# Kernel tuning notes

Hardware: AMD Instinct MI355X
Metric: run time of the kernel (lower is better)

Reference implementation:

```python
import jax, jax.numpy as jnp
import numpy as np

# ViT-B on the Lorentz hyperboloid (curvature C): points x = [x_time, x_space],
# x_time = sqrt(||x_space||^2 + C). All linear/conv/norm ops act on the space
# part and recompute time; residuals/attention-midpoints renormalize the full
# Lorentz vector back onto the hyperboloid.
B, IMG, P, CIN, D, H, L = 32, 224, 16, 3, 768, 12, 12
HD = D // H          # per-head space dim (64)
DFF = 2048           # swiglu hidden: int(2/3 * 4*768) aligned to 64
C = 1.0
EPS = 1e-6


def _time(xs):
    return jnp.sqrt(jnp.clip(jnp.sum(xs * xs, -1, keepdims=True) + C, EPS, None))


def _to_lorentz(xs):
    return jnp.concatenate([_time(xs), xs], -1)


def _project(z):
    # renormalize full Lorentz vector so <z,z>_L = -C
    zz = jnp.sum(z[..., 1:] ** 2, -1, keepdims=True) - z[..., :1] ** 2
    return z * (jnp.sqrt(C) / jnp.sqrt(jnp.clip(-zz, EPS, None)))


def _lorentz_ln(x, g, b):
    xs = x[..., 1:]
    mu = xs.mean(-1, keepdims=True)
    var = ((xs - mu) ** 2).mean(-1, keepdims=True)
    xs = (xs - mu) / jnp.sqrt(var + 1e-6) * g + b
    return _to_lorentz(xs)


def _lresnet(x, y, w):
    # Lorentzian weighted residual: midpoint of x and w*y, projected to manifold
    return _project(x + w * y)


def _rope_tables():
    # 2D axial rope over the 14x14 patch grid, identity rotation for 1 cls token
    n = IMG // P
    d4 = HD // 4
    inv = 1.0 / (100.0 ** (np.arange(d4) / d4))
    ang = np.arange(n)[:, None] * inv[None, :]            # [n, d4]
    ay = np.repeat(ang[:, None, :], n, axis=1)            # row angles
    ax = np.repeat(ang[None, :, :], n, axis=0)            # col angles
    a = np.concatenate([ay, ax], -1).reshape(n * n, HD // 2)
    cos = np.concatenate([np.ones((1, HD // 2)), np.cos(a)], 0)
    sin = np.concatenate([np.zeros((1, HD // 2)), np.sin(a)], 0)
    return jnp.asarray(cos, jnp.float32), jnp.asarray(sin, jnp.float32)


def _apply_rope(x, cos, sin):
    # x: [B,N,H,HD]; rotate consecutive pairs (complex multiply)
    xr = x.reshape(*x.shape[:-1], -1, 2)
    x0, x1 = xr[..., 0], xr[..., 1]
    c = cos[None, :, None, :]
    s = sin[None, :, None, :]
    out = jnp.stack([x0 * c - x1 * s, x0 * s + x1 * c], -1)
    return out.reshape(x.shape)


def _attention(x, Wq, Wk, Wv, Wo, cos, sin, scale):
    b, n, _ = x.shape
    xs = x[..., 1:]
    q = (xs @ Wq).reshape(b, n, H, HD)
    k = (xs @ Wk).reshape(b, n, H, HD)
    v = (xs @ Wv).reshape(b, n, H, HD)
    q = _apply_rope(q, cos, sin)
    k = _apply_rope(k, cos, sin)
    qt = _time(q)[..., 0]   # [B,N,H]
    kt = _time(k)[..., 0]
    # Lorentz inner product <q,k>_L = -q_t k_t + q_s . k_s
    inner = jnp.einsum('bnhd,bmhd->bhnm', q, k) - jnp.einsum('bnh,bmh->bhnm', qt, kt)
    attn = jax.nn.softmax((2.0 * C + 2.0 * inner) / scale, axis=-1)
    vf = jnp.concatenate([_time(v), v], -1)               # [B,M,H,HD+1]
    mid = jnp.einsum('bhnm,bmhe->bnhe', attn, vf)         # Lorentzian midpoint
    mid = _project(mid)
    out_s = mid[..., 1:].reshape(b, n, H * HD) @ Wo       # concat heads + proj
    return _to_lorentz(out_s)


def setup_inputs() -> dict:
    key = jax.random.key(0)
    ks = jax.random.split(key, 12)
    std = 0.02
    nrm = lambda k, shape: jax.random.normal(k, shape, jnp.float32) * std
    return {
        'x': jax.random.normal(ks[0], (B, CIN, IMG, IMG), jnp.float32),
        'cls_s': nrm(ks[1], (D - 1,)),
        'Wp': nrm(ks[2], (P, P, CIN + 1, D - 1)),         # HWIO conv kernel
        'ln1_g': jnp.ones((L, D - 1), jnp.float32),
        'ln1_b': jnp.zeros((L, D - 1), jnp.float32),
        'Wq': nrm(ks[3], (L, D - 1, H * HD)),
        'Wk': nrm(ks[4], (L, D - 1, H * HD)),
        'Wv': nrm(ks[5], (L, D - 1, H * HD)),
        'Wo': nrm(ks[6], (L, H * HD, D - 1)),
        'ln2_g': jnp.ones((L, D - 1), jnp.float32),
        'ln2_b': jnp.zeros((L, D - 1), jnp.float32),
        'W1': nrm(ks[7], (L, D - 1, DFF)),
        'W2': nrm(ks[8], (L, D - 1, DFF)),
        'W3': nrm(ks[9], (L, DFF, D - 1)),
        'wy1': jnp.ones((L,), jnp.float32),
        'wy2': jnp.ones((L,), jnp.float32),
        'lnf_g': jnp.ones((D - 1,), jnp.float32),
        'lnf_b': jnp.zeros((D - 1,), jnp.float32),
    }


def reference(x, cls_s, Wp, ln1_g, ln1_b, Wq, Wk, Wv, Wo, ln2_g, ln2_b,
              W1, W2, W3, wy1, wy2, lnf_g, lnf_b):
    b = x.shape[0]
    xs = jnp.transpose(x, (0, 2, 3, 1))                   # BHWC
    xl = _to_lorentz(xs)                                  # pixel-wise time channel
    feat = jax.lax.conv_general_dilated(
        xl, Wp, (P, P), 'VALID',
        dimension_numbers=('NHWC', 'HWIO', 'NHWC'))       # [B,14,14,D-1]
    tok = _to_lorentz(feat).reshape(b, -1, D)             # [B,196,D]
    cls = jnp.broadcast_to(_to_lorentz(cls_s)[None, None, :], (b, 1, D))
    tok = jnp.concatenate([cls, tok], 1)                  # [B,197,D]
    cos, sin = _rope_tables()
    scale = jnp.sqrt(jnp.asarray(H * HD, jnp.float32))
    for l in range(L):
        xn = _lorentz_ln(tok, ln1_g[l], ln1_b[l])
        a = _attention(xn, Wq[l], Wk[l], Wv[l], Wo[l], cos, sin, scale)
        tok = _lresnet(tok, a, wy1[l])
        xn = _lorentz_ln(tok, ln2_g[l], ln2_b[l])
        hs = xn[..., 1:]
        m = _to_lorentz((jax.nn.silu(hs @ W1[l]) * (hs @ W2[l])) @ W3[l])
        tok = _lresnet(tok, m, wy2[l])
    return _lorentz_ln(tok, lnf_g, lnf_b)
```

## Files before the change

kernel.cpp:

```cpp
#include <hip/hip_runtime.h>
#include <hip/hip_bf16.h>

typedef __attribute__((ext_vector_type(8))) short short8;
typedef __attribute__((ext_vector_type(4))) float f32x4;
typedef _Float16 f16x8 __attribute__((ext_vector_type(8)));

#define NLAYER 12
#define NTOK   6304
#define MPAD   6400
#define CONVM  6272

#define QELE     ((size_t)384*208*64)
#define VELE     ((size_t)384*80*232)

static constexpr size_t AL(size_t x){ return (x + 511) & ~(size_t)511; }
static constexpr size_t B_COS    = 0;
static constexpr size_t B_SIN    = AL(B_COS    + (size_t)197*32*4);
static constexpr size_t B_WPT    = AL(B_SIN    + (size_t)197*32*4);
static constexpr size_t B_APATCH = AL(B_WPT    + (size_t)768*1024*2);
static constexpr size_t B_WQKVT  = AL(B_APATCH + (size_t)CONVM*1024*2);
static constexpr size_t B_WOT    = AL(B_WQKVT  + (size_t)2304*768*2);
static constexpr size_t B_W12T   = AL(B_WOT    + (size_t)768*768*2);
static constexpr size_t B_W3T    = AL(B_W12T   + (size_t)4096*768*2);
static constexpr size_t B_TOK    = AL(B_W3T    + (size_t)768*2048*2);
static constexpr size_t B_ACTA   = AL(B_TOK    + (size_t)NTOK*768*4);
static constexpr size_t B_ACTB   = AL(B_ACTA   + (size_t)MPAD*768*2);
static constexpr size_t B_GOUT   = AL(B_ACTB   + (size_t)MPAD*2048*2);
static constexpr size_t B_QB     = AL(B_GOUT   + (size_t)MPAD*2304*4);
static constexpr size_t B_KB     = AL(B_QB     + QELE*2);
static constexpr size_t B_VT     = AL(B_KB     + QELE*2);
static constexpr size_t B_QTB    = AL(B_VT     + VELE*2);
static constexpr size_t B_KTB    = AL(B_QTB    + (size_t)384*208*4);
static constexpr size_t B_END    = AL(B_KTB    + (size_t)384*208*4);

typedef __attribute__((address_space(1))) unsigned int gu32;
typedef __attribute__((address_space(3))) unsigned int lu32;
__device__ __forceinline__ void gld16(const void* g, void* l) {
  __builtin_amdgcn_global_load_lds((const gu32*)g, (lu32*)l, 16, 0, 0);
}

__device__ __forceinline__ float bsum(float v, float* red) {
  #pragma unroll
  for (int m = 32; m; m >>= 1) v += __shfl_xor(v, m, 64);
  __syncthreads();
  if ((threadIdx.x & 63) == 0) red[threadIdx.x >> 6] = v;
  __syncthreads();
  return red[0] + red[1] + red[2] + red[3];
}

__device__ __forceinline__ ushort h_us(float v) {
  _Float16 h = (_Float16)v;
  return *(ushort*)&h;
}
__device__ __forceinline__ float us_f(ushort u) {
  return (float)*(const _Float16*)&u;
}

__global__ void k_rope_tab(float* __restrict__ cosb, float* __restrict__ sinb) {
  int idx = blockIdx.x * 256 + threadIdx.x;
  if (idx >= 197 * 32) return;
  int p = idx >> 5, j = idx & 31;
  float cv, sv;
  if (p == 0) { cv = 1.f; sv = 0.f; }
  else {
    int pp = p - 1;
    int iy = pp / 14, ix = pp - iy * 14;
    int pos = (j < 16) ? iy : ix;
    int f   = (j < 16) ? j  : j - 16;
    float inv = powf(100.f, -(float)f / 16.f);
    float a = (float)pos * inv;
    cv = cosf(a); sv = sinf(a);
  }
  cosb[idx] = cv; sinb[idx] = sv;
}

__device__ __forceinline__ void tpose_tile(const float* __restrict__ src, ushort* __restrict__ dst,
                                           int K, int N, int ldd, int imode, int tk, int tn) {
  __shared__ float ts[32][33];
  int t = threadIdx.x;
  int rr = t >> 3, c4 = (t & 7) * 4;
  int k0 = tk * 32, n0 = tn * 32;
  #pragma unroll
  for (int e = 0; e < 4; ++e) {
    int k = k0 + rr, n = n0 + c4 + e;
    ts[rr][c4 + e] = (k < K && n < N) ? src[(size_t)k * N + n] : 0.f;
  }
  __syncthreads();
  int c = n0 + rr;
  int drow = (imode == 0) ? c : (16 * (c >> 3) + (c & 7) + (imode == 2 ? 8 : 0));
  ushort4 o;
  #pragma unroll
  for (int e = 0; e < 4; ++e) {
    _Float16 hv = (_Float16)ts[c4 + e][rr];
    ((ushort*)&o)[e] = *(ushort*)&hv;
  }
  *(ushort4*)&dst[(size_t)drow * ldd + k0 + c4] = o;
}

__global__ __launch_bounds__(256) void k_tpose(const float* __restrict__ src, ushort* __restrict__ dst,
                                               int K, int N, int ktiles, int ldd) {
  int tk = blockIdx.x % ktiles, tn = blockIdx.x / ktiles;
  tpose_tile(src, dst, K, N, ldd, 0, tk, tn);
}

__global__ __launch_bounds__(256) void k_wprep(const float* __restrict__ Wq, const float* __restrict__ Wk,
                                               const float* __restrict__ Wv, const float* __restrict__ Wo,
                                               const float* __restrict__ W1, const float* __restrict__ W2,
                                               const float* __restrict__ W3,
                                               ushort* __restrict__ wqkvt, ushort* __restrict__ wot,
                                               ushort* __restrict__ w12t, ushort* __restrict__ w3t) {
  int tile = blockIdx.x;
  const float* src; ushort* dst;
  int K, N, ktiles, ldd, imode = 0, tl;
  if (tile < 2304) {
    int jb = tile / 576; tl = tile % 576;
    ktiles = 24; ldd = 768;
    if (jb == 0)      { src = Wq; dst = wqkvt;                 K = 767; N = 768; }
    else if (jb == 1) { src = Wk; dst = wqkvt + 768 * 768;     K = 767; N = 768; }
    else if (jb == 2) { src = Wv; dst = wqkvt + 2 * 768 * 768; K = 767; N = 768; }
    else              { src = Wo; dst = wot;                   K = 768; N = 767; }
  } else if (tile < 5376) {
    int jb = (tile - 2304) / 1536; tl = (tile - 2304) % 1536;
    ktiles = 24; ldd = 768; K = 767; N = 2048; dst = w12t;
    src = jb ? W2 : W1; imode = jb ? 2 : 1;
  } else {
    tl = tile - 5376; ktiles = 64; ldd = 2048; K = 2048; N = 767; src = W3; dst = w3t;
  }
  int tk = tl % ktiles, tn = tl / ktiles;
  tpose_tile(src, dst, K, N, ldd, imode, tk, tn);
}

__global__ __launch_bounds__(256) void k_im2col(const float* __restrict__ x, ushort* __restrict__ ap) {
  int r = blockIdx.x;
  int b = r / 196, pi = r - b * 196;
  int py = pi / 14, px = pi - py * 14;
  int t = threadIdx.x;
  int ph = t >> 4, pw = t & 15;
  int iy = py * 16 + ph, ix = px * 16 + pw;
  size_t base = ((size_t)b * 3 * 224 + iy) * 224 + ix;
  float x0 = x[base];
  float x1 = x[base + 224 * 224];
  float x2 = x[base + 2 * 224 * 224];
  float tv = sqrtf(fmaxf(x0 * x0 + x1 * x1 + x2 * x2 + 1.f, 1e-6f));
  size_t o = (size_t)r * 1024 + t * 4;
  ap[o] = h_us(tv); ap[o + 1] = h_us(x0); ap[o + 2] = h_us(x1); ap[o + 3] = h_us(x2);
}

template<int MODE>
__global__ __launch_bounds__(256) void k_gemmh(const ushort* __restrict__ A, const ushort* __restrict__ Bt,
                                               float* __restrict__ C, ushort* __restrict__ H,
                                               int N, int K,
                                               ushort* __restrict__ qbuf, ushort* __restrict__ kbuf,
                                               ushort* __restrict__ vtb,
                                               float* __restrict__ qtb, float* __restrict__ ktb,
                                               const float* __restrict__ cosb, const float* __restrict__ sinb) {
  __shared__ ushort sA[128 * 64];
  __shared__ ushort sB[128 * 64];
  int m0 = blockIdx.x * 128, n0 = blockIdx.y * 128;
  int t = threadIdx.x;
  int w = t >> 6, l = t & 63;
  int wm = (w >> 1) * 64, wn = (w & 1) * 64;
  int lr = l & 15, hi = l >> 4;
  f32x4 acc[4][4] = {};
  for (int k0 = 0; k0 < K; k0 += 64) {
    #pragma unroll
    for (int i = 0; i < 4; ++i) {
      int fl = i * 256 + t;
      int r = fl >> 3, c = fl & 7;
      int cs = c ^ (r & 7);
      gld16(&A[(size_t)(m0 + r) * K + k0 + cs * 8], &sA[fl * 8]);
      gld16(&Bt[(size_t)(n0 + r) * K + k0 + cs * 8], &sB[fl * 8]);
    }
    __syncthreads();
    f16x8 af[4][2], bfr[4][2];
    #pragma unroll
    for (int q = 0; q < 4; ++q) {
      int ra = wm + q * 16 + lr, rb = wn + q * 16 + lr;
      #pragma unroll
      for (int h = 0; h < 2; ++h) {
        af[q][h]  = *(const f16x8*)&sA[ra * 64 + ((h * 4 + hi) ^ (ra & 7)) * 8];
        bfr[q][h] = *(const f16x8*)&sB[rb * 64 + ((h * 4 + hi) ^ (rb & 7)) * 8];
      }
    }
    #pragma unroll
    for (int mi = 0; mi < 4; ++mi)
      #pragma unroll
      for (int ni = 0; ni < 4; ++ni) {
        acc[mi][ni] = __builtin_amdgcn_mfma_f32_16x16x32_f16(af[mi][0], bfr[ni][0], acc[mi][ni], 0, 0, 0);
        acc[mi][ni] = __builtin_amdgcn_mfma_f32_16x16x32_f16(af[mi][1], bfr[ni][1], acc[mi][ni], 0, 0, 0);
      }
    __syncthreads();
  }
  int rr = hi * 4, cc = lr;
  if (MODE == 1) {
    #pragma unroll
    for (int mi = 0; mi < 4; ++mi)
      #pragma unroll
      for (int ni = 0; ni < 4; ++ni) {
        int g = (n0 + wn + ni * 16) >> 4;
        #pragma unroll
        for (int j = 0; j < 4; ++j) {
          float v = acc[mi][ni][j];
          float p = __shfl_xor(v, 8);
          float u1 = (cc < 8) ? v : p;
          float u2 = (cc < 8) ? p : v;
          float hv = u1 / (1.f + __expf(-u1)) * u2;
          if (cc < 8)
            H[(size_t)(m0 + wm + mi * 16 + rr + j) * 2048 + g * 8 + cc] = h_us(hv);
        }
      }
  } else if (MODE == 2) {
    int secBase = n0 + wn;
    int sec = secBase / 768;
    int hh = (secBase - sec * 768) >> 6;
    #pragma unroll
    for (int mi = 0; mi < 4; ++mi) {
      float nrm[4];
      #pragma unroll
      for (int j = 0; j < 4; ++j) {
        float ss = 0.f;
        #pragma unroll
        for (int ni = 0; ni < 4; ++ni) ss += acc[mi][ni][j] * acc[mi][ni][j];
        #pragma unroll
        for (int m = 8; m; m >>= 1) ss += __shfl_xor(ss, m, 64);
        nrm[j] = sqrtf(fmaxf(ss + 1.f, 1e-6f));
      }
      #pragma unroll
      for (int j = 0; j < 4; ++j) {
        int m = m0 + wm + mi * 16 + rr + j;
        if (m < NTOK) {
          int b = m / 197, nn = m - b * 197;
          int bh = b * 12 + hh;
          if (sec == 2) {
            size_t vo = (size_t)bh * 80 * 232;
            if (lr == 0) vtb[vo + nn] = h_us(nrm[j]);
            #pragma unroll
            for (int ni = 0; ni < 4; ++ni) {
              int e = ni * 16 + lr;
              vtb[vo + (size_t)(1 + e) * 232 + nn] = h_us(acc[mi][ni][j]);
            }
          } else {
            float* tb = (sec == 0) ? qtb : ktb;
            ushort* ob = (sec == 0) ? qbuf : kbuf;
            if (lr == 0) tb[(size_t)bh * 208 + nn] = nrm[j];
            size_t rowb = ((size_t)bh * 208 + nn) * 64;
            #pragma unroll
            for (int ni = 0; ni < 4; ++ni) {
              int d = ni * 16 + lr;
              float v = acc[mi][ni][j];
              float p = __shfl_xor(v, 1);
              int j2 = d >> 1;
              float cz = cosb[nn * 32 + j2], sz = sinb[nn * 32 + j2];
              float rv = ((lr & 1) == 0) ? (v * cz - p * sz) : (p * sz + v * cz);
              ob[rowb + d] = h_us(rv);
            }
          }
        }
      }
    }
  } else if (MODE == 3) {
    #pragma unroll
    for (int mi = 0; mi < 4; ++mi)
      #pragma unroll
      for (int ni = 0; ni < 4; ++ni)
        #pragma unroll
        for (int j = 0; j < 4; ++j)
          H[(size_t)(m0 + wm + mi * 16 + rr + j) * N + (n0 + wn + ni * 16 + cc)] = h_us(acc[mi][ni][j]);
  } else {
    #pragma unroll
    for (int mi = 0; mi < 4; ++mi)
      #pragma unroll
      for (int ni = 0; ni < 4; ++ni)
        #pragma unroll
        for (int j = 0; j < 4; ++j)
          C[(size_t)(m0 + wm + mi * 16 + rr + j) * N + (n0 + wn + ni * 16 + cc)] = acc[mi][ni][j];
  }
}

__global__ __launch_bounds__(256) void k_build_tok(const float* __restrict__ feat, const float* __restrict__ cls,
                                                   float* __restrict__ tok) {
  __shared__ float red[8];
  int r = blockIdx.x;
  int b = r / 197, i = r - b * 197;
  int t = threadIdx.x;
  const float* src = (i == 0) ? cls : (feat + (size_t)(b * 196 + i - 1) * 768);
  float v0 = src[t], v1 = src[256 + t], v2 = (t < 255) ? src[512 + t] : 0.f;
  float qs = bsum(v0 * v0 + v1 * v1 + v2 * v2, red);
  float* tp = tok + (size_t)r * 768;
  if (t == 0) tp[0] = sqrtf(fmaxf(qs + 1.f, 1e-6f));
  tp[1 + t] = v0; tp[257 + t] = v1; if (t < 255) tp[513 + t] = v2;
}

__global__ __launch_bounds__(256) void k_ln(const float* __restrict__ tok, const float* __restrict__ g,
                                            const float* __restrict__ bb, ushort* __restrict__ out) {
  __shared__ float red[8];
  int r = blockIdx.x, t = threadIdx.x;
  const float* xp = tok + (size_t)r * 768;
  float v0 = xp[1 + t], v1 = xp[257 + t], v2 = (t < 255) ? xp[513 + t] : 0.f;
  float s = bsum(v0 + v1 + v2, red);
  float q = bsum(v0 * v0 + v1 * v1 + v2 * v2, red);
  float mu = s * (1.f / 767.f);
  float rstd = rsqrtf(fmaxf(q * (1.f / 767.f) - mu * mu, 0.f) + 1e-6f);
  size_t o = (size_t)r * 768;
  out[o + t]       = h_us((v0 - mu) * rstd * g[t]       + bb[t]);
  out[o + 256 + t] = h_us((v1 - mu) * rstd * g[256 + t] + bb[256 + t]);
  if (t < 255)
    out[o + 512 + t] = h_us((v2 - mu) * rstd * g[512 + t] + bb[512 + t]);
  if (t == 255) out[o + 767] = 0;
}

__global__ __launch_bounds__(128) void k_attn(const ushort* __restrict__ qbuf,
                                              const float* __restrict__ qtb,
                                              const ushort* __restrict__ kbuf,
                                              const float* __restrict__ ktb,
                                              const ushort* __restrict__ vtb,
                                              ushort* __restrict__ outa) {
  __shared__ ushort sK[208 * 72];
  __shared__ ushort sP[2][16 * 248];
  __shared__ float  sKt[208];
  int half = blockIdx.x, bh = blockIdx.y;
  int b = bh / 12, hd = bh - b * 12;
  int t = threadIdx.x, w = t >> 6, l = t & 63;
  const ushort* kg = kbuf + (size_t)bh * 208 * 64;
  for (int cks = t; cks < 1664; cks += 128) {
    int r = cks >> 3, c8 = (cks & 7) * 8;
    *(int4*)&sK[r * 72 + c8] = *(const int4*)&kg[r * 64 + c8];
  }
  for (int i = t; i < 208; i += 128) sKt[i] = ktb[(size_t)bh * 208 + i];
  __syncthreads();
  const ushort* qg = qbuf + (size_t)bh * 208 * 64;
  const ushort* vg = vtb + (size_t)bh * 80 * 232;
  const float invs = 0.03608439182435161f;
  int rt0 = half ? 7 : 0, rt1 = half ? 13 : 7;
  int lr = l & 15, hi4 = l >> 4;
  ushort* pw = &sP[w][0];
  for (int rt = rt0 + w; rt < rt1; rt += 2) {
    int qrow = (rt * 16 + lr) * 64 + hi4 * 8;
    f16x8 q0 = *(const f16x8*)&qg[qrow];
    f16x8 q1 = *(const f16x8*)&qg[qrow + 32];
    float qt4[4];
    #pragma unroll
    for (int j = 0; j < 4; ++j) qt4[j] = qtb[(size_t)bh * 208 + rt * 16 + hi4 * 4 + j];
    f32x4 acc[13];
    #pragma unroll
    for (int nt = 0; nt < 13; ++nt) {
      int kr = (nt * 16 + lr) * 72 + hi4 * 8;
      f16x8 k0 = *(const f16x8*)&sK[kr];
      f16x8 k1 = *(const f16x8*)&sK[kr + 32];
      acc[nt] = (f32x4){0.f, 0.f, 0.f, 0.f};
      acc[nt] = __builtin_amdgcn_mfma_f32_16x16x32_f16(q0, k0, acc[nt], 0, 0, 0);
      acc[nt] = __builtin_amdgcn_mfma_f32_16x16x32_f16(q1, k1, acc[nt], 0, 0, 0);
    }
    float mx[4] = {-1e30f, -1e30f, -1e30f, -1e30f};
    #pragma unroll
    for (int nt = 0; nt < 13; ++nt) {
      int cI = nt * 16 + lr;
      float ktc = sKt[cI];
      bool valid = (cI < 197);
      #pragma unroll
      for (int j = 0; j < 4; ++j) {
        float s = (2.f + 2.f * (acc[nt][j] - qt4[j] * ktc)) * invs;
        acc[nt][j] = s;
        if (valid) mx[j] = fmaxf(mx[j], s);
      }
    }
    #pragma unroll
    for (int j = 0; j < 4; ++j)
      #pragma unroll
      for (int m = 8; m; m >>= 1) mx[j] = fmaxf(mx[j], __shfl_xor(mx[j], m, 64));
    #pragma unroll
    for (int nt = 0; nt < 14; ++nt) {
      int cI = nt * 16 + lr;
      #pragma unroll
      for (int j = 0; j < 4; ++j) {
        float p = (nt < 13 && cI < 197) ? __expf(acc[nt][j] - mx[j]) : 0.f;
        pw[(hi4 * 4 + j) * 248 + cI] = h_us(p);
      }
    }
    f32x4 accO[5];
    #pragma unroll
    for (int et = 0; et < 5; ++et) accO[et] = (f32x4){0.f, 0.f, 0.f, 0.f};
    #pragma unroll
    for (int ks = 0; ks < 7; ++ks) {
      f16x8 pa = *(const f16x8*)&pw[lr * 248 + ks * 32 + hi4 * 8];
      #pragma unroll
      for (int et = 0; et < 5; ++et) {
        int er = et * 16 + lr;
        f16x8 bv = *(const f16x8*)&vg[(er > 64 ? 64 : er) * 232 + ks * 32 + hi4 * 8];
        accO[et] = __builtin_amdgcn_mfma_f32_16x16x32_f16(pa, bv, accO[et], 0, 0, 0);
      }
    }
    float ssq[4] = {0.f, 0.f, 0.f, 0.f};
    #pragma unroll
    for (int et = 0; et < 4; ++et)
      #pragma unroll
      for (int j = 0; j < 4; ++j) ssq[j] += accO[et][j] * accO[et][j];
    if (lr == 0) {
      #pragma unroll
      for (int j = 0; j < 4; ++j) ssq[j] += accO[4][j] * accO[4][j];
    }
    #pragma unroll
    for (int j = 0; j < 4; ++j)
      #pragma unroll
      for (int m = 8; m; m >>= 1) ssq[j] += __shfl_xor(ssq[j], m, 64);
    float rf4[4];
    #pragma unroll
    for (int j = 0; j < 4; ++j) {
      float o0 = __shfl(accO[0][j], (l & 48));
      rf4[j] = rsqrtf(fmaxf(2.f * o0 * o0 - ssq[j], 1e-6f));
    }
    #pragma unroll
    for (int et = 0; et < 5; ++et) {
      int e = et * 16 + lr;
      if (e == 0 || e >= 65) continue;
      #pragma unroll
      for (int j = 0; j < 4; ++j) {
        int n = rt * 16 + hi4 * 4 + j;
        if (n < 197)
          outa[((size_t)(b * 197 + n)) * 768 + hd * 64 + (e - 1)] = h_us(accO[et][j] * rf4[j]);
      }
    }
  }
}

template<int FIN>
__global__ __launch_bounds__(256) void k_resnet_ln(float* __restrict__ tok, const ushort* __restrict__ s,
                                                   const float* __restrict__ wyp, int l,
                                                   const float* __restrict__ g, const float* __restrict__ bb,
                                                   ushort* __restrict__ out16, float* __restrict__ out32) {
  __shared__ float red[8];
  __shared__ float bc[1];
  int r = blockIdx.x, t = threadIdx.x;
  float w = wyp[l];
  const ushort* sp = s + (size_t)r * 768;
  float* tp = tok + (size_t)r * 768;
  float s0 = us_f(sp[t]), s1 = us_f(sp[256 + t]), s2 = (t < 255) ? us_f(sp[512 + t]) : 0.f;
  float qs = bsum(s0 * s0 + s1 * s1 + s2 * s2, red);
  float at = sqrtf(fmaxf(qs + 1.f, 1e-6f));
  float z0 = tp[1 + t] + w * s0;
  float z1 = tp[257 + t] + w * s1;
  float z2 = (t < 255) ? (tp[513 + t] + w * s2) : 0.f;
  float zs = bsum(z0 * z0 + z1 * z1 + z2 * z2, red);
  if (t == 0) bc[0] = tp[0] + w * at;
  __syncthreads();
  float zt = bc[0];
  float rf = rsqrtf(fmaxf(zt * zt - zs, 1e-6f));
  float n0 = z0 * rf, n1 = z1 * rf, n2 = z2 * rf;
  tp[1 + t] = n0; tp[257 + t] = n1; if (t < 255) tp[513 + t] = n2;
  if (t == 0) tp[0] = zt * rf;
  float sm = bsum(n0 + n1 + n2, red);
  float sq = bsum(n0 * n0 + n1 * n1 + n2 * n2, red);
  float mu = sm * (1.f / 767.f);
  float rstd = rsqrtf(fmaxf(sq * (1.f / 767.f) - mu * mu, 0.f) + 1e-6f);
  float y0 = (n0 - mu) * rstd * g[t] + bb[t];
  float y1 = (n1 - mu) * rstd * g[256 + t] + bb[256 + t];
  float y2 = (t < 255) ? ((n2 - mu) * rstd * g[512 + t] + bb[512 + t]) : 0.f;
  if (FIN) {
    float qq = bsum(y0 * y0 + y1 * y1 + y2 * y2, red);
    float* op = out32 + (size_t)r * 768;
    op[1 + t] = y0; op[257 + t] = y1; if (t < 255) op[513 + t] = y2;
    if (t == 0) op[0] = sqrtf(fmaxf(qq + 1.f, 1e-6f));
  } else {
    size_t o = (size_t)r * 768;
    out16[o + t] = h_us(y0);
    out16[o + 256 + t] = h_us(y1);
    if (t < 255) out16[o + 512 + t] = h_us(y2);
    if (t == 255) out16[o + 767] = 0;
  }
}

extern "C" void kernel_launch(void* const* d_in, const int* in_sizes, int n_in,
                              void* d_out, int out_size, void* d_ws, size_t ws_size,
                              hipStream_t stream) {
  const float* x     = (const float*)d_in[0];
  const float* cls_s = (const float*)d_in[1];
  const float* Wp    = (const float*)d_in[2];
  const float* ln1g  = (const float*)d_in[3];
  const float* ln1b  = (const float*)d_in[4];
  const float* Wq    = (const float*)d_in[5];
  const float* Wk    = (const float*)d_in[6];
  const float* Wv    = (const float*)d_in[7];
  const float* Wo    = (const float*)d_in[8];
  const float* ln2g  = (const float*)d_in[9];
  const float* ln2b  = (const float*)d_in[10];
  const float* W1    = (const float*)d_in[11];
  const float* W2    = (const float*)d_in[12];
  const float* W3    = (const float*)d_in[13];
  const float* wy1   = (const float*)d_in[14];
  const float* wy2   = (const float*)d_in[15];
  const float* lnfg  = (const float*)d_in[16];
  const float* lnfb  = (const float*)d_in[17];

  if (ws_size < B_END) return;

  char* ws = (char*)d_ws;
  float*  cosb   = (float*)(ws + B_COS);
  float*  sinb   = (float*)(ws + B_SIN);
  ushort* wpt    = (ushort*)(ws + B_WPT);
  ushort* apatch = (ushort*)(ws + B_APATCH);
  ushort* wqkvt  = (ushort*)(ws + B_WQKVT);
  ushort* wot    = (ushort*)(ws + B_WOT);
  ushort* w12t   = (ushort*)(ws + B_W12T);
  ushort* w3t    = (ushort*)(ws + B_W3T);
  float*  tok    = (float*)(ws + B_TOK);
  ushort* acta   = (ushort*)(ws + B_ACTA);
  ushort* actb   = (ushort*)(ws + B_ACTB);
  float*  gout   = (float*)(ws + B_GOUT);
  ushort* gouth  = (ushort*)(ws + B_GOUT);
  ushort* qbuf   = (ushort*)(ws + B_QB);
  ushort* kbuf   = (ushort*)(ws + B_KB);
  ushort* vtb    = (ushort*)(ws + B_VT);
  float*  qtb    = (float*)(ws + B_QTB);
  float*  ktb    = (float*)(ws + B_KTB);

  hipMemsetAsync(vtb, 0, VELE * 2, stream);

  k_rope_tab<<<25, 256, 0, stream>>>(cosb, sinb);
  k_tpose<<<32 * 24, 256, 0, stream>>>(Wp, wpt, 1024, 767, 32, 1024);
  k_im2col<<<CONVM, 256, 0, stream>>>(x, apatch);
  k_gemmh<0><<<dim3(49, 6), 256, 0, stream>>>(apatch, wpt, gout, nullptr, 768, 1024,
                                              nullptr, nullptr, nullptr, nullptr, nullptr, nullptr, nullptr);
  k_build_tok<<<NTOK, 256, 0, stream>>>(gout, cls_s, tok);
  k_ln<<<NTOK, 256, 0, stream>>>(tok, ln1g, ln1b, acta);

  for (int l = 0; l < NLAYER; ++l) {
    k_wprep<<<6912, 256, 0, stream>>>(Wq + (size_t)l * 767 * 768, Wk + (size_t)l * 767 * 768,
                                      Wv + (size_t)l * 767 * 768, Wo + (size_t)l * 768 * 767,
                                      W1 + (size_t)l * 767 * 2048, W2 + (size_t)l * 767 * 2048,
                                      W3 + (size_t)l * 2048 * 767, wqkvt, wot, w12t, w3t);

    k_gemmh<2><<<dim3(50, 18), 256, 0, stream>>>(acta, wqkvt, nullptr, nullptr, 2304, 768,
                                                 qbuf, kbuf, vtb, qtb, ktb, cosb, sinb);
    k_attn<<<dim3(2, 384), 128, 0, stream>>>(qbuf, qtb, kbuf, ktb, vtb, acta);
    k_gemmh<3><<<dim3(50, 6), 256, 0, stream>>>(acta, wot, nullptr, gouth, 768, 768,
                                                nullptr, nullptr, nullptr, nullptr, nullptr, nullptr, nullptr);
    k_resnet_ln<0><<<NTOK, 256, 0, stream>>>(tok, gouth, wy1, l,
                                             ln2g + (size_t)l * 767, ln2b + (size_t)l * 767, acta, nullptr);

    k_gemmh<1><<<dim3(50, 32), 256, 0, stream>>>(acta, w12t, nullptr, actb, 4096, 768,
                                                 nullptr, nullptr, nullptr, nullptr, nullptr, nullptr, nullptr);
    k_gemmh<3><<<dim3(50, 6), 256, 0, stream>>>(actb, w3t, nullptr, gouth, 768, 2048,
                                                nullptr, nullptr, nullptr, nullptr, nullptr, nullptr, nullptr);
    if (l < NLAYER - 1)
      k_resnet_ln<0><<<NTOK, 256, 0, stream>>>(tok, gouth, wy2, l,
                                               ln1g + (size_t)(l + 1) * 767, ln1b + (size_t)(l + 1) * 767,
                                               acta, nullptr);
    else
      k_resnet_ln<1><<<NTOK, 256, 0, stream>>>(tok, gouth, wy2, l, lnfg, lnfb, nullptr, (float*)d_out);
  }
}
```

Before: 3.338 ms.

## Add 256x256 double-buffered GEMM kernel for QKV and SwiGLU projections

After: 3.284 ms. About the same (-1.6%).

```diff
diff --git a/kernel.cpp b/kernel.cpp
--- a/kernel.cpp
+++ b/kernel.cpp
@@ -149,11 +149,7 @@
 template<int MODE>
 __global__ __launch_bounds__(256) void k_gemmh(const ushort* __restrict__ A, const ushort* __restrict__ Bt,
                                                float* __restrict__ C, ushort* __restrict__ H,
-                                               int N, int K,
-                                               ushort* __restrict__ qbuf, ushort* __restrict__ kbuf,
-                                               ushort* __restrict__ vtb,
-                                               float* __restrict__ qtb, float* __restrict__ ktb,
-                                               const float* __restrict__ cosb, const float* __restrict__ sinb) {
+                                               int N, int K) {
   __shared__ ushort sA[128 * 64];
   __shared__ ushort sB[128 * 64];
   int m0 = blockIdx.x * 128, n0 = blockIdx.y * 128;
@@ -192,12 +188,136 @@
     __syncthreads();
   }
   int rr = hi * 4, cc = lr;
+  if (MODE == 3) {
+    #pragma unroll
+    for (int mi = 0; mi < 4; ++mi)
+      #pragma unroll
+      for (int ni = 0; ni < 4; ++ni)
+        #pragma unroll
+        for (int j = 0; j < 4; ++j)
+          H[(size_t)(m0 + wm + mi * 16 + rr + j) * N + (n0 + wn + ni * 16 + cc)] = h_us(acc[mi][ni][j]);
+  } else {
+    #pragma unroll
+    for (int mi = 0; mi < 4; ++mi)
+      #pragma unroll
+      for (int ni = 0; ni < 4; ++ni)
+        #pragma unroll
+        for (int j = 0; j < 4; ++j)
+          C[(size_t)(m0 + wm + mi * 16 + rr + j) * N + (n0 + wn + ni * 16 + cc)] = acc[mi][ni][j];
+  }
+}
+
+template<int MODE>
+__global__ __launch_bounds__(512, 2) void k_g256(const ushort* __restrict__ A, const ushort* __restrict__ Bt,
+                                                 ushort* __restrict__ H, int N, int K,
+                                                 ushort* __restrict__ qbuf, ushort* __restrict__ kbuf,
+                                                 ushort* __restrict__ vtb,
+                                                 float* __restrict__ qtb, float* __restrict__ ktb,
+                                                 const float* __restrict__ cosb, const float* __restrict__ sinb) {
+  __shared__ ushort sA[2][2][256 * 32];
+  __shared__ ushort sB[2][2][256 * 32];
+  const int t = threadIdx.x;
+  const int w = t >> 6, l = t & 63;
+  const int wr = w >> 2, wc = w & 3;
+  const int lr = l & 15, hi4 = l >> 4;
+  const int m0 = blockIdx.x * 256, n0 = blockIdx.y * 256;
+
+  auto stageA = [&](int kt, int kh, int buf) {
+    #pragma unroll
+    for (int ii = 0; ii < 2; ++ii) {
+      int q = ii * 512 + t;
+      int r = q >> 2, ci = q & 3;
+      gld16(&A[(size_t)(m0 + r) * K + kt * 64 + kh * 32 + ((ci ^ (r & 3)) * 8)], &sA[buf][kh][q * 8]);
+    }
+  };
+  auto stageB = [&](int kt, int kh, int buf) {
+    #pragma unroll
+    for (int ii = 0; ii < 2; ++ii) {
+      int q = ii * 512 + t;
+      int r = q >> 2, ci = q & 3;
+      gld16(&Bt[(size_t)(n0 + r) * K + kt * 64 + kh * 32 + ((ci ^ (r & 3)) * 8)], &sB[buf][kh][q * 8]);
+    }
+  };
+
+  f32x4 acc[8][4] = {};
+  auto ldA = [&](int buf, int ks, int G, f16x8* fr) {
+    #pragma unroll
+    for (int mi = 0; mi < 4; ++mi) {
+      int r = wr * 128 + (G * 4 + mi) * 16 + lr;
+      fr[mi] = *(const f16x8*)&sA[buf][ks][(r * 4 + (hi4 ^ (r & 3))) * 8];
+    }
+  };
+  auto ldB = [&](int buf, int ks, f16x8* fr) {
+    #pragma unroll
+    for (int ni = 0; ni < 4; ++ni) {
+      int r = wc * 64 + ni * 16 + lr;
+      fr[ni] = *(const f16x8*)&sB[buf][ks][(r * 4 + (hi4 ^ (r & 3))) * 8];
+    }
+  };
+  auto mmaG = [&](int G, f16x8* a, f16x8* b) {
+    __builtin_amdgcn_s_setprio(1);
+    #pragma unroll
+    for (int mi = 0; mi < 4; ++mi)
+      #pragma unroll
+      for (int ni = 0; ni < 4; ++ni)
+        acc[G * 4 + mi][ni] = __builtin_amdgcn_mfma_f32_16x16x32_f16(a[mi], b[ni], acc[G * 4 + mi][ni], 0, 0, 0);
+    __builtin_amdgcn_s_setprio(0);
+  };
+
+  const int NT = K >> 6;
+  const int NI = NT >> 1;
+  stageA(0, 0, 0); stageB(0, 0, 0); stageA(0, 1, 0); stageB(0, 1, 0);
+
+  for (int i = 0; i < NI; ++i) {
+    const int T1 = 2 * i + 1, T2 = 2 * i + 2;
+    const bool last = (i == NI - 1);
+    f16x8 a0[4], a1[4], b0[4], b1[4];
+    asm volatile("s_waitcnt vmcnt(4)" ::: "memory");
+    __builtin_amdgcn_sched_barrier(0);
+    __builtin_amdgcn_s_barrier();
+    ldA(0, 0, 0, a0); ldB(0, 0, b0);
+    stageA(T1, 0, 1);
+    mmaG(0, a0, b0);
+    ldA(0, 0, 1, a1);
+    stageB(T1, 0, 1);
+    mmaG(1, a1, b0);
+    asm volatile("s_waitcnt vmcnt(4)" ::: "memory");
+    __builtin_amdgcn_sched_barrier(0);
+    __builtin_amdgcn_s_barrier();
+    ldA(0, 1, 0, a0); ldB(0, 1, b1);
+    stageA(T1, 1, 1);
+    mmaG(0, a0, b1);
+    ldA(0, 1, 1, a1);
+    stageB(T1, 1, 1);
+    mmaG(1, a1, b1);
+    asm volatile("s_waitcnt vmcnt(4)" ::: "memory");
+    __builtin_amdgcn_sched_barrier(0);
+    __builtin_amdgcn_s_barrier();
+    ldA(1, 0, 0, a0); ldB(1, 0, b0);
+    if (!last) stageA(T2, 0, 0);
+    mmaG(0, a0, b0);
+    ldA(1, 0, 1, a1);
+    if (!last) stageB(T2, 0, 0);
+    mmaG(1, a1, b0);
+    if (last) { asm volatile("s_waitcnt vmcnt(0)" ::: "memory"); }
+    else      { asm volatile("s_waitcnt vmcnt(4)" ::: "memory"); }
+    __builtin_amdgcn_sched_barrier(0);
+    __builtin_amdgcn_s_barrier();
+    ldA(1, 1, 0, a0); ldB(1, 1, b1);
+    if (!last) stageA(T2, 1, 0);
+    mmaG(0, a0, b1);
+    ldA(1, 1, 1, a1);
+    if (!last) stageB(T2, 1, 0);
+    mmaG(1, a1, b1);
+  }
+
   if (MODE == 1) {
-    #pragma unroll
-    for (int mi = 0; mi < 4; ++mi)
+    int cc = lr;
+    #pragma unroll
+    for (int mi = 0; mi < 8; ++mi)
       #pragma unroll
       for (int ni = 0; ni < 4; ++ni) {
-        int g = (n0 + wn + ni * 16) >> 4;
+        int g = (n0 + wc * 64 + ni * 16) >> 4;
         #pragma unroll
         for (int j = 0; j < 4; ++j) {
           float v = acc[mi][ni][j];
@@ -206,15 +326,15 @@
           float u2 = (cc < 8) ? p : v;
           float hv = u1 / (1.f + __expf(-u1)) * u2;
           if (cc < 8)
-            H[(size_t)(m0 + wm + mi * 16 + rr + j) * 2048 + g * 8 + cc] = h_us(hv);
+            H[(size_t)(m0 + wr * 128 + mi * 16 + hi4 * 4 + j) * 2048 + g * 8 + cc] = h_us(hv);
         }
       }
   } else if (MODE == 2) {
-    int secBase = n0 + wn;
+    int secBase = n0 + wc * 64;
     int sec = secBase / 768;
     int hh = (secBase - sec * 768) >> 6;
     #pragma unroll
-    for (int mi = 0; mi < 4; ++mi) {
+    for (int mi = 0; mi < 8; ++mi) {
       float nrm[4];
       #pragma unroll
       for (int j = 0; j < 4; ++j) {
@@ -227,7 +347,7 @@
       }
       #pragma unroll
       for (int j = 0; j < 4; ++j) {
-        int m = m0 + wm + mi * 16 + rr + j;
+        int m = m0 + wr * 128 + mi * 16 + hi4 * 4 + j;
         if (m < NTOK) {
           int b = m / 197, nn = m - b * 197;
           int bh = b * 12 + hh;
@@ -258,22 +378,6 @@
         }
       }
     }
-  } else if (MODE == 3) {
-    #pragma unroll
-    for (int mi = 0; mi < 4; ++mi)
-      #pragma unroll
-      for (int ni = 0; ni < 4; ++ni)
-        #pragma unroll
-        for (int j = 0; j < 4; ++j)
-          H[(size_t)(m0 + wm + mi * 16 + rr + j) * N + (n0 + wn + ni * 16 + cc)] = h_us(acc[mi][ni][j]);
-  } else {
-    #pragma unroll
-    for (int mi = 0; mi < 4; ++mi)
-      #pragma unroll
-      for (int ni = 0; ni < 4; ++ni)
-        #pragma unroll
-        for (int j = 0; j < 4; ++j)
-          C[(size_t)(m0 + wm + mi * 16 + rr + j) * N + (n0 + wn + ni * 16 + cc)] = acc[mi][ni][j];
   }
 }
 
@@ -518,8 +622,7 @@
   k_rope_tab<<<25, 256, 0, stream>>>(cosb, sinb);
   k_tpose<<<32 * 24, 256, 0, stream>>>(Wp, wpt, 1024, 767, 32, 1024);
   k_im2col<<<CONVM, 256, 0, stream>>>(x, apatch);
-  k_gemmh<0><<<dim3(49, 6), 256, 0, stream>>>(apatch, wpt, gout, nullptr, 768, 1024,
-                                              nullptr, nullptr, nullptr, nullptr, nullptr, nullptr, nullptr);
+  k_gemmh<0><<<dim3(49, 6), 256, 0, stream>>>(apatch, wpt, gout, nullptr, 768, 1024);
   k_build_tok<<<NTOK, 256, 0, stream>>>(gout, cls_s, tok);
   k_ln<<<NTOK, 256, 0, stream>>>(tok, ln1g, ln1b, acta);
 
@@ -529,18 +632,16 @@
                                       W1 + (size_t)l * 767 * 2048, W2 + (size_t)l * 767 * 2048,
                                       W3 + (size_t)l * 2048 * 767, wqkvt, wot, w12t, w3t);
 
-    k_gemmh<2><<<dim3(50, 18), 256, 0, stream>>>(acta, wqkvt, nullptr, nullptr, 2304, 768,
-                                                 qbuf, kbuf, vtb, qtb, ktb, cosb, sinb);
+    k_g256<2><<<dim3(25, 9), 512, 0, stream>>>(acta, wqkvt, nullptr, 2304, 768,
+                                               qbuf, kbuf, vtb, qtb, ktb, cosb, sinb);
     k_attn<<<dim3(2, 384), 128, 0, stream>>>(qbuf, qtb, kbuf, ktb, vtb, acta);
-    k_gemmh<3><<<dim3(50, 6), 256, 0, stream>>>(acta, wot, nullptr, gouth, 768, 768,
-                                                nullptr, nullptr, nullptr, nullptr, nullptr, nullptr, nullptr);
+    k_gemmh<3><<<dim3(50, 6), 256, 0, stream>>>(acta, wot, nullptr, gouth, 768, 768);
     k_resnet_ln<0><<<NTOK, 256, 0, stream>>>(tok, gouth, wy1, l,
                                              ln2g + (size_t)l * 767, ln2b + (size_t)l * 767, acta, nullptr);
 
-    k_gemmh<1><<<dim3(50, 32), 256, 0, stream>>>(acta, w12t, nullptr, actb, 4096, 768,
-                                                 nullptr, nullptr, nullptr, nullptr, nullptr, nullptr, nullptr);
-    k_gemmh<3><<<dim3(50, 6), 256, 0, stream>>>(actb, w3t, nullptr, gouth, 768, 2048,
+    k_g256<1><<<dim3(25, 16), 512, 0, stream>>>(acta, w12t, actb, 4096, 768,
                                                 nullptr, nullptr, nullptr, nullptr, nullptr, nullptr, nullptr);
+    k_gemmh<3><<<dim3(50, 6), 256, 0, stream>>>(actb, w3t, nullptr, gouth, 768, 2048);
     if (l < NLAYER - 1)
       k_resnet_ln<0><<<NTOK, 256, 0, stream>>>(tok, gouth, wy2, l,
                                                ln1g + (size_t)(l + 1) * 767, ln1b + (size_t)(l + 1) * 767,
```
